# Optimization experiments

Hardware: AMD Instinct MI355X
Metric: run time of the kernel (lower is better)

## Reference

```python
import jax, jax.numpy as jnp
import numpy as np

B, DIM, HW = 2, 2, 512
HID, OUT, NL = 64, 3, 4  # no_layers=4 -> NL+1 filters


def _linear2d(w, b, inp):
    # 1x1 conv: w [o,i], inp [b,i,x,y] -> [b,o,x,y]
    return jnp.einsum('oi,bixy->boxy', w, inp) + b[None, :, None, None]


def _gabor_filter(x, w, b, mu_l, gamma_l, theta_l):
    # Rotated gaussian window. x: [B,2,H,W]
    ang = 2.0 * jnp.pi * theta_l  # [C]
    c, s = jnp.cos(ang), jnp.sin(ang)
    # rotation_matrix: rows [[cos, sin], [-sin, cos]] per channel -> [C,2,2]
    R = jnp.stack([jnp.stack([c, s], -1), jnp.stack([-s, c], -1)], -2)
    diff = x[:, None] - mu_l[None, :, :, None, None]          # [B,C,2,H,W]
    rot = jnp.einsum('coi,bcixy->bcoxy', R, diff)              # [B,C,2,H,W]
    g = jnp.exp(-0.5 * jnp.sum((gamma_l[None, :, :, None, None] * rot) ** 2, axis=2))
    return g * jnp.sin(_linear2d(w, b, x))                     # [B,C,H,W]


def setup_inputs() -> dict:
    key = jax.random.key(0)
    ks = jax.random.split(key, 10)
    inv_sqrt_hid = 1.0 / np.sqrt(HID)
    return {
        'x': jax.random.uniform(ks[0], (B, DIM, HW, HW), jnp.float32, -1.0, 1.0),
        'filt_w': jax.random.normal(ks[1], (NL + 1, HID, DIM), jnp.float32) * 0.1,
        'filt_b': jax.random.uniform(ks[2], (NL + 1, HID), jnp.float32, -np.pi, np.pi),
        'mu': jax.random.uniform(ks[3], (NL + 1, HID, DIM), jnp.float32, -1.0, 1.0),
        'gamma': jax.random.uniform(ks[4], (NL + 1, HID, DIM), jnp.float32, 0.5, 6.0),
        'theta': jax.random.uniform(ks[5], (NL + 1, HID), jnp.float32),
        'lin_w': jax.random.uniform(ks[6], (NL, HID, HID), jnp.float32, -inv_sqrt_hid, inv_sqrt_hid),
        'lin_b': jax.random.normal(ks[7], (NL, HID), jnp.float32) * 0.01,
        'out_w': jax.random.normal(ks[8], (OUT, HID), jnp.float32) * inv_sqrt_hid,
        'out_b': jax.random.normal(ks[9], (OUT,), jnp.float32) * 0.01,
    }


def reference(x, filt_w, filt_b, mu, gamma, theta, lin_w, lin_b, out_w, out_b):
    out = _gabor_filter(x, filt_w[0], filt_b[0], mu[0], gamma[0], theta[0])
    for i in range(1, NL + 1):
        lin = _linear2d(lin_w[i - 1], lin_b[i - 1], out)
        out = _gabor_filter(x, filt_w[i], filt_b[i], mu[i], gamma[i], theta[i]) * lin
    return _linear2d(out_w, out_b, out)  # [B,OUT,H,W]
```

## Files before the change

kernel.cpp:

```cpp
#include <hip/hip_runtime.h>
#include <hip/hip_bf16.h>
#include <math.h>

#define HW2 262144
#define TWO_PI     6.28318530717958647693f
#define INV_TWO_PI 0.15915494309189533577f
#define LOG2E      1.44269504088896340736f

typedef float  f32x4  __attribute__((ext_vector_type(4)));
typedef float  f32x8  __attribute__((ext_vector_type(8)));
typedef short  s16x8  __attribute__((ext_vector_type(8)));
typedef short  s16x4  __attribute__((ext_vector_type(4)));
typedef unsigned short ushort_t;

template <int I> struct ic { static constexpr int v = I; };
template <int I, int N, typename F>
__device__ __forceinline__ void sfor(F&& f) {
    if constexpr (I < N) { f(ic<I>{}); sfor<I + 1, N>(f); }
}

__device__ __forceinline__ ushort_t bf16_hi(float v) {
    __hip_bfloat16 h = __float2bfloat16(v);
    return __builtin_bit_cast(ushort_t, h);
}
__device__ __forceinline__ float bf16_tof(ushort_t u) {
    unsigned int x = ((unsigned int)u) << 16;
    return __builtin_bit_cast(float, x);
}

#define WS_WHI  10240
#define WS_WLO  43008
#define WS_WOH  75776
#define WS_WOL  77824

__global__ void gabor_pre(const float* __restrict__ filt_w,
                          const float* __restrict__ filt_b,
                          const float* __restrict__ mu,
                          const float* __restrict__ gamma,
                          const float* __restrict__ theta,
                          const float* __restrict__ lin_w,
                          const float* __restrict__ out_w,
                          float* __restrict__ pcq,
                          ushort_t* __restrict__ whi, ushort_t* __restrict__ wlo,
                          ushort_t* __restrict__ wouthi, ushort_t* __restrict__ woutlo) {
    int t = blockIdx.x * 256 + threadIdx.x;
    if (t < 320) {
        int i = t;
        float ang = TWO_PI * theta[i];
        float cs = cosf(ang), sn = sinf(ang);
        float g0 = gamma[i*2+0], g1 = gamma[i*2+1];
        float g0s = g0*g0, g1s = g1*g1;
        float cs2 = cs*cs, sn2 = sn*sn;
        float* o = pcq + i*8;
        o[0] = -0.5f * LOG2E * (g0s*cs2 + g1s*sn2);
        o[1] = -LOG2E * (cs*sn*(g0s - g1s));
        o[2] = -0.5f * LOG2E * (g0s*sn2 + g1s*cs2);
        o[3] = mu[i*2+0];
        o[4] = mu[i*2+1];
        o[5] = filt_w[i*2+0] * INV_TWO_PI;
        o[6] = filt_w[i*2+1] * INV_TWO_PI;
        o[7] = filt_b[i] * INV_TWO_PI;
    } else if (t < 320 + 16384) {
        int i = t - 320;
        float w = lin_w[i];
        ushort_t h = bf16_hi(w);
        whi[i] = h;
        wlo[i] = bf16_hi(w - bf16_tof(h));
    } else if (t < 320 + 16384 + 1024) {
        int i = t - (320 + 16384);
        int m = i >> 6;
        float w = (m < 3) ? out_w[i] : 0.0f;
        ushort_t h = bf16_hi(w);
        wouthi[i] = h;
        woutlo[i] = bf16_hi(w - bf16_tof(h));
    }
}

__device__ __forceinline__ float geval(f32x4 qa, f32x4 qb, float x0, float x1) {
    float d0 = x0 - qa[3];
    float d1 = x1 - qb[0];
    float t  = fmaf(qa[0]*d0, d0, fmaf(qa[1]*d0, d1, qa[2]*d1*d1));
    float e  = __builtin_amdgcn_exp2f(t);
    float sa = fmaf(qb[1], x0, fmaf(qb[2], x1, qb[3]));
    return e * __builtin_amdgcn_sinf(sa);
}

__global__ __launch_bounds__(64, 2) void gabor_mfma(
    const float* __restrict__ x, const float* __restrict__ lin_b,
    const float* __restrict__ out_b, const float* __restrict__ pcq,
    const ushort_t* __restrict__ whi, const ushort_t* __restrict__ wlo,
    const ushort_t* __restrict__ wouthi, const ushort_t* __restrict__ woutlo,
    float* __restrict__ out) {
    __shared__ __attribute__((aligned(16))) unsigned char hbuf[16384];
    const int lane = threadIdx.x;
    const int g    = lane >> 4;
    const int lm   = lane & 15;
    const int base = blockIdx.x * 64;

    f32x4 x0v, x1v;
    int pixo[4];
    sfor<0, 4>([&](auto NI) {
        int P  = base + NI.v*16 + lm;
        int bb = P >> 18, pix = P & (HW2 - 1);
        const float* xb = x + bb*(2*HW2) + pix;
        x0v[NI.v] = xb[0];
        x1v[NI.v] = xb[HW2];
        pixo[NI.v] = bb*(3*HW2) + pix;
    });

    sfor<0, 2>([&](auto KC) {
        f32x8 vv[4];
        sfor<0, 8>([&](auto J) {
            const float* q = pcq + (KC.v*32 + g*8 + J.v)*8;
            f32x4 qa = *(const f32x4*)q, qb = *(const f32x4*)(q + 4);
            sfor<0, 4>([&](auto NI) {
                vv[NI.v][J.v] = geval(qa, qb, x0v[NI.v], x1v[NI.v]);
            });
        });
        sfor<0, 4>([&](auto NI) {
            s16x8 fh, fl;
            sfor<0, 8>([&](auto J) {
                float v = vv[NI.v][J.v];
                ushort_t h = bf16_hi(v);
                fh[J.v] = (short)h;
                fl[J.v] = (short)bf16_hi(v - bf16_tof(h));
            });
            int px  = NI.v*16 + lm;
            int blk = (4*KC.v + g) ^ (px & 7);
            char* p0 = (char*)hbuf + px*128 + blk*16;
            *(s16x8*)(p0)        = fh;
            *(s16x8*)(p0 + 8192) = fl;
        });
    });

#pragma unroll 1
    for (int l = 1; l <= 4; ++l) {
        __syncthreads();
        const ushort_t* whl = whi + (l-1)*4096;
        const ushort_t* wll = wlo + (l-1)*4096;
        const float*    bv  = lin_b + (l-1)*64;
        f32x4 acc[4][4];
        sfor<0, 4>([&](auto MI) {
            f32x4 bias = *(const f32x4*)(bv + MI.v*16 + 4*g);
            sfor<0, 4>([&](auto NI) { acc[MI.v][NI.v] = bias; });
        });
        sfor<0, 2>([&](auto KC) {
            s16x8 bh[4], bl[4];
            sfor<0, 4>([&](auto NI) {
                int px  = NI.v*16 + lm;
                int blk = (4*KC.v + g) ^ (px & 7);
                const char* p0 = (const char*)hbuf + px*128 + blk*16;
                bh[NI.v] = *(const s16x8*)(p0);
                bl[NI.v] = *(const s16x8*)(p0 + 8192);
            });
            sfor<0, 4>([&](auto MI) {
                int off = (MI.v*16 + lm)*64 + KC.v*32 + g*8;
                s16x8 ah = *(const s16x8*)(whl + off);
                s16x8 al = *(const s16x8*)(wll + off);
                sfor<0, 4>([&](auto NI) {
                    f32x4 a = acc[MI.v][NI.v];
                    a = __builtin_amdgcn_mfma_f32_16x16x32_bf16(ah, bh[NI.v], a, 0, 0, 0);
                    a = __builtin_amdgcn_mfma_f32_16x16x32_bf16(ah, bl[NI.v], a, 0, 0, 0);
                    a = __builtin_amdgcn_mfma_f32_16x16x32_bf16(al, bh[NI.v], a, 0, 0, 0);
                    a = __builtin_amdgcn_mfma_f32_16x16x32_bf16(al, bl[NI.v], a, 0, 0, 0);
                    acc[MI.v][NI.v] = a;
                });
            });
        });
        __syncthreads();
        const float* pcl = pcq + l*512;
        sfor<0, 4>([&](auto MI) {
            f32x4 vo[4];
            sfor<0, 4>([&](auto R) {
                const float* q = pcl + (MI.v*16 + 4*g + R.v)*8;
                f32x4 qa = *(const f32x4*)q, qb = *(const f32x4*)(q + 4);
                sfor<0, 4>([&](auto NI) {
                    vo[NI.v][R.v] = geval(qa, qb, x0v[NI.v], x1v[NI.v])
                                    * acc[MI.v][NI.v][R.v];
                });
            });
            sfor<0, 4>([&](auto NI) {
                s16x4 fh, fl;
                sfor<0, 4>([&](auto R) {
                    float v = vo[NI.v][R.v];
                    ushort_t h = bf16_hi(v);
                    fh[R.v] = (short)h;
                    fl[R.v] = (short)bf16_hi(v - bf16_tof(h));
                });
                int px  = NI.v*16 + lm;
                int blk = (2*MI.v + (g >> 1)) ^ (px & 7);
                char* p0 = (char*)hbuf + px*128 + blk*16 + (g & 1)*8;
                *(s16x4*)(p0)        = fh;
                *(s16x4*)(p0 + 8192) = fl;
            });
        });
    }

    __syncthreads();
    f32x4 ao[4];
    sfor<0, 4>([&](auto NI) { ao[NI.v] = (f32x4)(0.0f); });
    sfor<0, 2>([&](auto KC) {
        s16x8 bh[4], bl[4];
        sfor<0, 4>([&](auto NI) {
            int px  = NI.v*16 + lm;
            int blk = (4*KC.v + g) ^ (px & 7);
            const char* p0 = (const char*)hbuf + px*128 + blk*16;
            bh[NI.v] = *(const s16x8*)(p0);
            bl[NI.v] = *(const s16x8*)(p0 + 8192);
        });
        int off = lm*64 + KC.v*32 + g*8;
        s16x8 ah = *(const s16x8*)(wouthi + off);
        s16x8 al = *(const s16x8*)(woutlo + off);
        sfor<0, 4>([&](auto NI) {
            f32x4 a = ao[NI.v];
            a = __builtin_amdgcn_mfma_f32_16x16x32_bf16(ah, bh[NI.v], a, 0, 0, 0);
            a = __builtin_amdgcn_mfma_f32_16x16x32_bf16(ah, bl[NI.v], a, 0, 0, 0);
            a = __builtin_amdgcn_mfma_f32_16x16x32_bf16(al, bh[NI.v], a, 0, 0, 0);
            a = __builtin_amdgcn_mfma_f32_16x16x32_bf16(al, bl[NI.v], a, 0, 0, 0);
            ao[NI.v] = a;
        });
    });
    if (lane < 16) {
        float ob0 = out_b[0], ob1 = out_b[1], ob2 = out_b[2];
        sfor<0, 4>([&](auto NI) {
            float* po = out + pixo[NI.v];
            po[0]     = ao[NI.v][0] + ob0;
            po[HW2]   = ao[NI.v][1] + ob1;
            po[2*HW2] = ao[NI.v][2] + ob2;
        });
    }
}

extern "C" void kernel_launch(void* const* d_in, const int* in_sizes, int n_in,
                              void* d_out, int out_size, void* d_ws, size_t ws_size,
                              hipStream_t stream) {
    const float* x      = (const float*)d_in[0];
    const float* filt_w = (const float*)d_in[1];
    const float* filt_b = (const float*)d_in[2];
    const float* mu     = (const float*)d_in[3];
    const float* gamma  = (const float*)d_in[4];
    const float* theta  = (const float*)d_in[5];
    const float* lin_w  = (const float*)d_in[6];
    const float* lin_b  = (const float*)d_in[7];
    const float* out_w  = (const float*)d_in[8];
    const float* out_b  = (const float*)d_in[9];

    char* ws = (char*)d_ws;
    float*    pcq    = (float*)ws;
    ushort_t* whi    = (ushort_t*)(ws + WS_WHI);
    ushort_t* wlo    = (ushort_t*)(ws + WS_WLO);
    ushort_t* wouthi = (ushort_t*)(ws + WS_WOH);
    ushort_t* woutlo = (ushort_t*)(ws + WS_WOL);

    gabor_pre<<<70, 256, 0, stream>>>(filt_w, filt_b, mu, gamma, theta,
                                      lin_w, out_w, pcq, whi, wlo, wouthi, woutlo);
    gabor_mfma<<<8192, 64, 0, stream>>>(x, lin_b, out_b, pcq, whi, wlo,
                                        wouthi, woutlo, (float*)d_out);
}
```

Before: 149.0 us.

## Expand Gaussian quadratic, drop lo*lo MFMA term, use two-wave blocks

```diff
diff --git a/kernel.cpp b/kernel.cpp
--- a/kernel.cpp
+++ b/kernel.cpp
@@ -28,10 +28,10 @@
     return __builtin_bit_cast(float, x);
 }
 
-#define WS_WHI  10240
-#define WS_WLO  43008
-#define WS_WOH  75776
-#define WS_WOL  77824
+#define WS_WHI  15360
+#define WS_WLO  48128
+#define WS_WOH  80896
+#define WS_WOL  82944
 
 __global__ void gabor_pre(const float* __restrict__ filt_w,
                           const float* __restrict__ filt_b,
@@ -51,15 +51,19 @@
         float g0 = gamma[i*2+0], g1 = gamma[i*2+1];
         float g0s = g0*g0, g1s = g1*g1;
         float cs2 = cs*cs, sn2 = sn*sn;
-        float* o = pcq + i*8;
-        o[0] = -0.5f * LOG2E * (g0s*cs2 + g1s*sn2);
-        o[1] = -LOG2E * (cs*sn*(g0s - g1s));
-        o[2] = -0.5f * LOG2E * (g0s*sn2 + g1s*cs2);
-        o[3] = mu[i*2+0];
-        o[4] = mu[i*2+1];
-        o[5] = filt_w[i*2+0] * INV_TWO_PI;
-        o[6] = filt_w[i*2+1] * INV_TWO_PI;
-        o[7] = filt_b[i] * INV_TWO_PI;
+        float A = -0.5f * LOG2E * (g0s*cs2 + g1s*sn2);
+        float B = -LOG2E * (cs*sn*(g0s - g1s));
+        float C = -0.5f * LOG2E * (g0s*sn2 + g1s*cs2);
+        float m0 = mu[i*2+0], m1 = mu[i*2+1];
+        float* o = pcq + i*12;
+        o[0] = A;  o[1] = B;  o[2] = C;
+        o[3] = -(2.0f*A*m0 + B*m1);
+        o[4] = -(B*m0 + 2.0f*C*m1);
+        o[5] = A*m0*m0 + B*m0*m1 + C*m1*m1;
+        o[6] = filt_w[i*2+0] * INV_TWO_PI;
+        o[7] = filt_w[i*2+1] * INV_TWO_PI;
+        o[8] = filt_b[i] * INV_TWO_PI;
+        o[9] = 0.0f; o[10] = 0.0f; o[11] = 0.0f;
     } else if (t < 320 + 16384) {
         int i = t - 320;
         float w = lin_w[i];
@@ -76,45 +80,51 @@
     }
 }
 
-__device__ __forceinline__ float geval(f32x4 qa, f32x4 qb, float x0, float x1) {
-    float d0 = x0 - qa[3];
-    float d1 = x1 - qb[0];
-    float t  = fmaf(qa[0]*d0, d0, fmaf(qa[1]*d0, d1, qa[2]*d1*d1));
+__device__ __forceinline__ float geval(f32x4 qa, f32x4 qb, float br,
+                                       float x0, float x1,
+                                       float x02, float x11, float x12) {
+    float t = fmaf(qa[0], x02, fmaf(qa[1], x11,
+              fmaf(qa[2], x12, fmaf(qa[3], x0, fmaf(qb[0], x1, qb[1])))));
     float e  = __builtin_amdgcn_exp2f(t);
-    float sa = fmaf(qb[1], x0, fmaf(qb[2], x1, qb[3]));
+    float sa = fmaf(qb[2], x0, fmaf(qb[3], x1, br));
     return e * __builtin_amdgcn_sinf(sa);
 }
 
-__global__ __launch_bounds__(64, 2) void gabor_mfma(
+__global__ __launch_bounds__(128, 2) void gabor_mfma(
     const float* __restrict__ x, const float* __restrict__ lin_b,
     const float* __restrict__ out_b, const float* __restrict__ pcq,
     const ushort_t* __restrict__ whi, const ushort_t* __restrict__ wlo,
     const ushort_t* __restrict__ wouthi, const ushort_t* __restrict__ woutlo,
     float* __restrict__ out) {
-    __shared__ __attribute__((aligned(16))) unsigned char hbuf[16384];
-    const int lane = threadIdx.x;
+    __shared__ __attribute__((aligned(16))) unsigned char hbuf2[2][16384];
+    const int lane = threadIdx.x & 63;
+    const int wid  = threadIdx.x >> 6;
     const int g    = lane >> 4;
     const int lm   = lane & 15;
-    const int base = blockIdx.x * 64;
-
-    f32x4 x0v, x1v;
+    const int base = blockIdx.x * 128 + wid * 64;
+    unsigned char* hbuf = hbuf2[wid];
+
+    f32x4 x0v, x1v, x02v, x11v, x12v;
     int pixo[4];
     sfor<0, 4>([&](auto NI) {
         int P  = base + NI.v*16 + lm;
         int bb = P >> 18, pix = P & (HW2 - 1);
         const float* xb = x + bb*(2*HW2) + pix;
-        x0v[NI.v] = xb[0];
-        x1v[NI.v] = xb[HW2];
+        float a = xb[0], b = xb[HW2];
+        x0v[NI.v] = a;  x1v[NI.v] = b;
+        x02v[NI.v] = a*a;  x11v[NI.v] = a*b;  x12v[NI.v] = b*b;
         pixo[NI.v] = bb*(3*HW2) + pix;
     });
 
     sfor<0, 2>([&](auto KC) {
         f32x8 vv[4];
         sfor<0, 8>([&](auto J) {
-            const float* q = pcq + (KC.v*32 + g*8 + J.v)*8;
+            const float* q = pcq + (KC.v*32 + g*8 + J.v)*12;
             f32x4 qa = *(const f32x4*)q, qb = *(const f32x4*)(q + 4);
+            float br = q[8];
             sfor<0, 4>([&](auto NI) {
-                vv[NI.v][J.v] = geval(qa, qb, x0v[NI.v], x1v[NI.v]);
+                vv[NI.v][J.v] = geval(qa, qb, br, x0v[NI.v], x1v[NI.v],
+                                      x02v[NI.v], x11v[NI.v], x12v[NI.v]);
             });
         });
         sfor<0, 4>([&](auto NI) {
@@ -162,20 +172,21 @@
                     a = __builtin_amdgcn_mfma_f32_16x16x32_bf16(ah, bh[NI.v], a, 0, 0, 0);
                     a = __builtin_amdgcn_mfma_f32_16x16x32_bf16(ah, bl[NI.v], a, 0, 0, 0);
                     a = __builtin_amdgcn_mfma_f32_16x16x32_bf16(al, bh[NI.v], a, 0, 0, 0);
-                    a = __builtin_amdgcn_mfma_f32_16x16x32_bf16(al, bl[NI.v], a, 0, 0, 0);
                     acc[MI.v][NI.v] = a;
                 });
             });
         });
         __syncthreads();
-        const float* pcl = pcq + l*512;
+        const float* pcl = pcq + l*768;
         sfor<0, 4>([&](auto MI) {
             f32x4 vo[4];
             sfor<0, 4>([&](auto R) {
-                const float* q = pcl + (MI.v*16 + 4*g + R.v)*8;
+                const float* q = pcl + (MI.v*16 + 4*g + R.v)*12;
                 f32x4 qa = *(const f32x4*)q, qb = *(const f32x4*)(q + 4);
+                float br = q[8];
                 sfor<0, 4>([&](auto NI) {
-                    vo[NI.v][R.v] = geval(qa, qb, x0v[NI.v], x1v[NI.v])
+                    vo[NI.v][R.v] = geval(qa, qb, br, x0v[NI.v], x1v[NI.v],
+                                          x02v[NI.v], x11v[NI.v], x12v[NI.v])
                                     * acc[MI.v][NI.v][R.v];
                 });
             });
@@ -216,7 +227,6 @@
             a = __builtin_amdgcn_mfma_f32_16x16x32_bf16(ah, bh[NI.v], a, 0, 0, 0);
             a = __builtin_amdgcn_mfma_f32_16x16x32_bf16(ah, bl[NI.v], a, 0, 0, 0);
             a = __builtin_amdgcn_mfma_f32_16x16x32_bf16(al, bh[NI.v], a, 0, 0, 0);
-            a = __builtin_amdgcn_mfma_f32_16x16x32_bf16(al, bl[NI.v], a, 0, 0, 0);
             ao[NI.v] = a;
         });
     });
@@ -254,6 +264,6 @@
 
     gabor_pre<<<70, 256, 0, stream>>>(filt_w, filt_b, mu, gamma, theta,
                                       lin_w, out_w, pcq, whi, wlo, wouthi, woutlo);
-    gabor_mfma<<<8192, 64, 0, stream>>>(x, lin_b, out_b, pcq, whi, wlo,
-                                        wouthi, woutlo, (float*)d_out);
-}
+    gabor_mfma<<<4096, 128, 0, stream>>>(x, lin_b, out_b, pcq, whi, wlo,
+                                         wouthi, woutlo, (float*)d_out);
+}
```

After: 158.2 us. 1.06x slower.
